# Performance work log

Measured on AMD Instinct MI355X. Metric: run time of the kernel, lower is better.

Reference implementation:

```python
import jax, jax.numpy as jnp
import numpy as np
from jax import lax

D_MODEL = 768
EXPAND = 2
D_INNER = D_MODEL * EXPAND  # 1536
N_STATE = 16
DT_RANK = D_INNER // 16  # 96
K_CONV = 4
B, L = 2, 1024


def setup_inputs() -> dict:
    key = jax.random.key(0)
    ks = jax.random.split(key, 20)
    s = lambda i, shape, scale=0.02: jax.random.normal(ks[i], shape, dtype=jnp.float32) * scale
    # dt_proj bias init (inverse softplus of dt in [0.001, 0.1])
    def dt_bias(k):
        dt = jnp.exp(jax.random.uniform(k, (D_INNER,)) * (np.log(0.1) - np.log(0.001)) + np.log(0.001))
        return dt + jnp.log(-jnp.expm1(-dt))
    A_log = jnp.log(jnp.arange(1, N_STATE + 1, dtype=jnp.float32))[None, :] * jnp.ones((D_INNER, 1), jnp.float32)
    inp = {
        "u": jax.random.normal(ks[0], (B, L, D_MODEL), dtype=jnp.float32),
        "norm_w": jnp.ones((D_MODEL,), jnp.float32),
        "norm_b": jnp.zeros((D_MODEL,), jnp.float32),
        "fwd_in_w": s(1, (2 * D_INNER, D_MODEL)),
        "fwd_conv_w": s(2, (D_INNER, 1, K_CONV), 0.1),
        "fwd_conv_b": jnp.zeros((D_INNER,), jnp.float32),
        "fwd_A_log": A_log,
        "fwd_xproj_w": s(3, (DT_RANK + 2 * N_STATE, D_INNER)),
        "fwd_dt_w": s(4, (D_INNER, DT_RANK)),
        "fwd_dt_b": dt_bias(ks[5]),
        "fwd_D": jnp.ones((D_INNER,), jnp.float32),
        "bwd_in_w": s(6, (2 * D_INNER, D_MODEL)),
        "bwd_conv_w": s(7, (D_INNER, 1, K_CONV), 0.1),
        "bwd_conv_b": jnp.zeros((D_INNER,), jnp.float32),
        "bwd_A_log": A_log,
        "bwd_xproj_w": s(8, (DT_RANK + 2 * N_STATE, D_INNER)),
        "bwd_dt_w": s(9, (D_INNER, DT_RANK)),
        "bwd_dt_b": dt_bias(ks[10]),
        "bwd_D": jnp.ones((D_INNER,), jnp.float32),
        "out_w": s(11, (D_MODEL, 2 * D_INNER)),
    }
    return inp


def _layernorm(x, w, b, eps=1e-5):
    mu = jnp.mean(x, axis=-1, keepdims=True)
    var = jnp.mean(jnp.square(x - mu), axis=-1, keepdims=True)
    return (x - mu) * lax.rsqrt(var + eps) * w + b


def _dw_causal_conv(x, w, b):
    # x: (B, L, D); torch Conv1d(pad=k-1, groups=D) then trim to L == left-pad causal conv
    xc = jnp.transpose(x, (0, 2, 1))  # (B, D, L)
    y = lax.conv_general_dilated(xc, w, window_strides=(1,),
                                 padding=[(K_CONV - 1, 0)],
                                 feature_group_count=D_INNER,
                                 dimension_numbers=('NCH', 'OIH', 'NCH'))
    return jnp.transpose(y + b[None, :, None], (0, 2, 1))


def _ssm(x, A_log, xproj_w, dt_w, dt_b, Dp):
    # x: (B, L, D)
    x_dbl = x @ xproj_w.T  # (B, L, dt_rank + 2N)
    dt_raw = x_dbl[..., :DT_RANK]
    B_sel = x_dbl[..., DT_RANK:DT_RANK + N_STATE]   # (B, L, N)
    C_sel = x_dbl[..., DT_RANK + N_STATE:]           # (B, L, N)
    dt = jax.nn.softplus(dt_raw @ dt_w.T + dt_b)      # (B, L, D)
    A = -jnp.exp(A_log)                               # (D, N)
    A_bar = jnp.exp(dt[..., None] * A)                # (B, L, D, N)
    Bu = (dt * x)[..., None] * B_sel[:, :, None, :]   # (B, L, D, N)
    # linear recurrence h_t = A_bar_t * h_{t-1} + Bu_t via associative scan
    def combine(c1, c2):
        a1, b1 = c1
        a2, b2 = c2
        return a1 * a2, a2 * b1 + b2
    _, h = lax.associative_scan(combine, (A_bar, Bu), axis=1)
    y = jnp.einsum('bldn,bln->bld', h, C_sel)
    return y + x * Dp


def _branch(u, in_w, conv_w, conv_b, A_log, xproj_w, dt_w, dt_b, Dp, reverse):
    if reverse:
        u = u[:, ::-1]
    xz = u @ in_w.T
    x, z = xz[..., :D_INNER], xz[..., D_INNER:]
    x = jax.nn.silu(_dw_causal_conv(x, conv_w, conv_b))
    x = _ssm(x, A_log, xproj_w, dt_w, dt_b, Dp)
    x = x * jax.nn.silu(z)
    if reverse:
        x = x[:, ::-1]
    return x


def reference(u, norm_w, norm_b,
              fwd_in_w, fwd_conv_w, fwd_conv_b, fwd_A_log, fwd_xproj_w, fwd_dt_w, fwd_dt_b, fwd_D,
              bwd_in_w, bwd_conv_w, bwd_conv_b, bwd_A_log, bwd_xproj_w, bwd_dt_w, bwd_dt_b, bwd_D,
              out_w):
    residual = u
    un = _layernorm(u, norm_w, norm_b)
    x_fwd = _branch(un, fwd_in_w, fwd_conv_w, fwd_conv_b, fwd_A_log, fwd_xproj_w, fwd_dt_w, fwd_dt_b, fwd_D, False)
    x_bwd = _branch(un, bwd_in_w, bwd_conv_w, bwd_conv_b, bwd_A_log, bwd_xproj_w, bwd_dt_w, bwd_dt_b, bwd_D, True)
    x = jnp.concatenate([x_fwd, x_bwd], axis=-1) @ out_w.T
    return x + residual
```

## Files before the change

kernel.cpp:

```cpp
#include <hip/hip_runtime.h>
#include <hip/hip_bf16.h>

#define D_MODEL 768
#define D_INNER 1536
#define N_STATE 16
#define DT_RANK 96
#define KCONV   4
#define Bv      2
#define Lv      1024
#define MROWS   (Bv*Lv)

typedef __attribute__((ext_vector_type(8))) short bf16x8;
typedef __attribute__((ext_vector_type(4))) float f32x4;

__device__ __forceinline__ void gll16(const void* g, void* l) {
    __builtin_amdgcn_global_load_lds(
        (const __attribute__((address_space(1))) void*)g,
        (__attribute__((address_space(3))) void*)l, 16, 0, 0);
}

__device__ __forceinline__ unsigned short f2bf(float f) {
    unsigned u = __builtin_bit_cast(unsigned, f);
    u += 0x7fffu + ((u >> 16) & 1u);
    return (unsigned short)(u >> 16);
}

__global__ __launch_bounds__(256)
void ln_kernel(const float* __restrict__ u, const float* __restrict__ w,
               const float* __restrict__ bvec, unsigned short* __restrict__ o)
{
    int row = blockIdx.x;
    const float* x = u + (size_t)row * D_MODEL;
    int t = threadIdx.x;
    float v0 = x[t], v1 = x[t + 256], v2 = x[t + 512];
    float s  = v0 + v1 + v2;
    float s2 = v0*v0 + v1*v1 + v2*v2;
    for (int off = 32; off; off >>= 1) {
        s  += __shfl_down(s, off);
        s2 += __shfl_down(s2, off);
    }
    __shared__ float rs[4], rs2[4];
    __shared__ float mu_s, rstd_s;
    int wid = t >> 6, lane = t & 63;
    if (lane == 0) { rs[wid] = s; rs2[wid] = s2; }
    __syncthreads();
    if (t == 0) {
        float S  = rs[0] + rs[1] + rs[2] + rs[3];
        float S2 = rs2[0] + rs2[1] + rs2[2] + rs2[3];
        float mu = S / (float)D_MODEL;
        float var = S2 / (float)D_MODEL - mu * mu;
        mu_s = mu;
        rstd_s = rsqrtf(var + 1e-5f);
    }
    __syncthreads();
    float mu = mu_s, r = rstd_s;
    unsigned short* orow = o + (size_t)row * D_MODEL;
    orow[t]       = f2bf((v0 - mu) * r * w[t]       + bvec[t]);
    orow[t + 256] = f2bf((v1 - mu) * r * w[t + 256] + bvec[t + 256]);
    orow[t + 512] = f2bf((v2 - mu) * r * w[t + 512] + bvec[t + 512]);
}

__global__ __launch_bounds__(256)
void f2b(const float* __restrict__ in, unsigned short* __restrict__ o, int n4)
{
    int i = blockIdx.x * 256 + threadIdx.x;
    if (i < n4) {
        float4 v = ((const float4*)in)[i];
        ushort4 r;
        r.x = f2bf(v.x); r.y = f2bf(v.y); r.z = f2bf(v.z); r.w = f2bf(v.w);
        ((ushort4*)o)[i] = r;
    }
}

__global__ __launch_bounds__(256)
void gemm_mfma(const unsigned short* __restrict__ A, int revA, int Lr,
               const unsigned short* __restrict__ W,
               const float* __restrict__ res,
               float* __restrict__ C,
               int M, int N, int K)
{
    __shared__ unsigned short As[128 * 32];
    __shared__ unsigned short Bs[128 * 32];
    const int tid = threadIdx.x;
    const int m0 = blockIdx.y * 128, n0 = blockIdx.x * 128;
    const int lane = tid & 63;
    const int w  = tid >> 6;
    const int wr = w >> 1, wc = w & 1;
    const int lm = lane & 15, lk = lane >> 4;

    const int srow = tid >> 2;
    const int skq  = (tid & 3) * 8;
    int arow0 = m0 + srow, arow1 = m0 + srow + 64;
    if (revA) {
        arow0 = (arow0 / Lr) * Lr + (Lr - 1 - arow0 % Lr);
        arow1 = (arow1 / Lr) * Lr + (Lr - 1 - arow1 % Lr);
    }
    const unsigned short* a0 = A + (size_t)arow0 * K + skq;
    const unsigned short* a1 = A + (size_t)arow1 * K + skq;
    const unsigned short* w0 = W + (size_t)(n0 + srow) * K + skq;
    const unsigned short* w1 = W + (size_t)(n0 + srow + 64) * K + skq;

    f32x4 acc[4][4] = {};

    for (int k0 = 0; k0 < K; k0 += 32) {
        __syncthreads();
        gll16(a0 + k0, &As[tid * 8]);
        gll16(a1 + k0, &As[2048 + tid * 8]);
        gll16(w0 + k0, &Bs[tid * 8]);
        gll16(w1 + k0, &Bs[2048 + tid * 8]);
        __syncthreads();

        bf16x8 af[4], bfr[4];
        #pragma unroll
        for (int i = 0; i < 4; i++) {
            af[i]  = *(const bf16x8*)&As[(wr * 64 + i * 16 + lm) * 32 + lk * 8];
            bfr[i] = *(const bf16x8*)&Bs[(wc * 64 + i * 16 + lm) * 32 + lk * 8];
        }
        #pragma unroll
        for (int i = 0; i < 4; i++)
            #pragma unroll
            for (int j = 0; j < 4; j++)
                acc[i][j] = __builtin_amdgcn_mfma_f32_16x16x32_bf16(af[i], bfr[j], acc[i][j], 0, 0, 0);
    }

    #pragma unroll
    for (int i = 0; i < 4; i++) {
        #pragma unroll
        for (int j = 0; j < 4; j++) {
            int row = m0 + wr * 64 + i * 16 + lk * 4;
            int col = n0 + wc * 64 + j * 16 + lm;
            #pragma unroll
            for (int r = 0; r < 4; r++) {
                float v = acc[i][j][r];
                if (res) v += res[(size_t)(row + r) * N + col];
                C[(size_t)(row + r) * N + col] = v;
            }
        }
    }
}

__global__ __launch_bounds__(256)
void conv_silu(const float* __restrict__ xz, const float* __restrict__ w,
               const float* __restrict__ bias, float* __restrict__ xo,
               unsigned short* __restrict__ xbf)
{
    int t  = blockIdx.x * 256 + threadIdx.x;
    int d  = t % D_INNER;
    int lc = (t / D_INNER) % (Lv / 8);
    int b  = t / (D_INNER * (Lv / 8));
    int l0 = lc * 8;
    const float* src = xz + (size_t)b * Lv * (2 * D_INNER) + d;
    float w0 = w[d*4], w1 = w[d*4+1], w2 = w[d*4+2], w3 = w[d*4+3];
    float bb = bias[d];
    float v[11];
    #pragma unroll
    for (int j = 0; j < 11; j++) {
        int l = l0 - 3 + j;
        v[j] = (l >= 0) ? src[(size_t)l * (2 * D_INNER)] : 0.f;
    }
    size_t base = ((size_t)b * Lv + l0) * D_INNER + d;
    #pragma unroll
    for (int j = 0; j < 8; j++) {
        float a = bb + w0*v[j] + w1*v[j+1] + w2*v[j+2] + w3*v[j+3];
        a = a / (1.f + __expf(-a));
        xo[base + (size_t)j * D_INNER] = a;
        xbf[base + (size_t)j * D_INNER] = f2bf(a);
    }
}

__global__ __launch_bounds__(256)
void gemm_bt(const float* __restrict__ A, int lda, int aoff, int revA, int Lr,
             const float* __restrict__ W, int ldw,
             const float* __restrict__ bias, int act,
             const float* __restrict__ res, int ldres,
             float* __restrict__ C, int ldc,
             int M, int N, int K)
{
    __shared__ float As[16][64];
    __shared__ float Ws[16][64];
    const int t  = threadIdx.x;
    const int m0 = blockIdx.y * 64, n0 = blockIdx.x * 64;
    const int lr = t >> 2, kq = t & 3;
    int am = m0 + lr;
    if (revA) { int b = am / Lr, l = am % Lr; am = b * Lr + (Lr - 1 - l); }
    const float* Ap = A + (size_t)am * lda + aoff + kq * 4;
    const float* Wp = W + (size_t)(n0 + lr) * ldw + kq * 4;
    const int ty = t >> 4, tx = t & 15;
    float acc[4][4] = {};
    for (int k0 = 0; k0 < K; k0 += 16) {
        float4 av = *(const float4*)(Ap + k0);
        float4 wv = *(const float4*)(Wp + k0);
        __syncthreads();
        As[kq*4+0][lr] = av.x; As[kq*4+1][lr] = av.y;
        As[kq*4+2][lr] = av.z; As[kq*4+3][lr] = av.w;
        Ws[kq*4+0][lr] = wv.x; Ws[kq*4+1][lr] = wv.y;
        Ws[kq*4+2][lr] = wv.z; Ws[kq*4+3][lr] = wv.w;
        __syncthreads();
        #pragma unroll
        for (int k = 0; k < 16; k++) {
            float4 ra = *(const float4*)&As[k][ty << 2];
            float4 rw = *(const float4*)&Ws[k][tx << 2];
            float a4[4] = {ra.x, ra.y, ra.z, ra.w};
            float w4[4] = {rw.x, rw.y, rw.z, rw.w};
            #pragma unroll
            for (int i = 0; i < 4; i++)
                #pragma unroll
                for (int j = 0; j < 4; j++)
                    acc[i][j] = fmaf(a4[i], w4[j], acc[i][j]);
        }
    }
    #pragma unroll
    for (int i = 0; i < 4; i++) {
        int row = m0 + (ty << 2) + i;
        #pragma unroll
        for (int j = 0; j < 4; j++) {
            int col = n0 + (tx << 2) + j;
            float v = acc[i][j];
            if (bias) v += bias[col];
            if (act == 2) v = (v > 20.f) ? v : log1pf(__expf(v));
            if (res)  v += res[(size_t)row * ldres + col];
            C[(size_t)row * ldc + col] = v;
        }
    }
}

#define SCH  64
#define SNC  (Lv/SCH)
#define PADL 68

template<int CTRL>
__device__ __forceinline__ float dpp_ror_add(float v) {
    int vi = __builtin_bit_cast(int, v);
    int mv = __builtin_amdgcn_update_dpp(vi, vi, CTRL, 0xf, 0xf, true);
    return v + __builtin_bit_cast(float, mv);
}

__global__ __launch_bounds__(128)
void scan_kernel(const float* __restrict__ xF,  const float* __restrict__ dtF,
                 const float* __restrict__ xdF, const float* __restrict__ xzF,
                 const float* __restrict__ AlF, const float* __restrict__ DFp,
                 const float* __restrict__ xB,  const float* __restrict__ dtB,
                 const float* __restrict__ xdB, const float* __restrict__ xzB,
                 const float* __restrict__ AlB, const float* __restrict__ DBp,
                 unsigned short* __restrict__ ycat)
{
    const int br = blockIdx.z;
    const int bb = blockIdx.y;
    const int d0 = blockIdx.x * 8;

    const float* x    = br ? xB  : xF;
    const float* dt   = br ? dtB : dtF;
    const float* xd   = br ? xdB : xdF;
    const float* xz   = br ? xzB : xzF;
    const float* Alog = br ? AlB : AlF;
    const float* Dp   = br ? DBp : DFp;

    __shared__ float xs [2][8][PADL];
    __shared__ float dts[2][8][PADL];
    __shared__ float zs [2][8][PADL];
    __shared__ float Bss[2][16][PADL];
    __shared__ float Css[2][16][PADL];

    const int t = threadIdx.x;
    const int n = t & 15, dloc = t >> 4;

    const float* xg  = x  + (size_t)bb * Lv * D_INNER + d0;
    const float* dtg = dt + (size_t)bb * Lv * D_INNER + d0;
    const float* zg  = xz + (size_t)bb * Lv * (2*D_INNER) + D_INNER + d0;
    const float* bcg = xd + (size_t)bb * Lv * 128;

    const int sl = t >> 1, sdq = (t & 1) * 4;
    const int bl0 = t >> 2,         bq0 = (t & 3) * 4;
    const int bl1 = (t + 128) >> 2, bq1 = ((t + 128) & 3) * 4;

    f32x4 rx, rdt, rz, rb0, rb1, rc0, rc1;

    #define LOADG(c) do {                                                        \
        int l0_ = (c) * SCH;                                                     \
        rx  = *(const f32x4*)(xg  + (size_t)(l0_ + sl) * D_INNER     + sdq);     \
        rdt = *(const f32x4*)(dtg + (size_t)(l0_ + sl) * D_INNER     + sdq);     \
        rz  = *(const f32x4*)(zg  + (size_t)(l0_ + sl) * (2*D_INNER) + sdq);     \
        rb0 = *(const f32x4*)(bcg + (size_t)(l0_ + bl0) * 128 + DT_RANK           + bq0); \
        rb1 = *(const f32x4*)(bcg + (size_t)(l0_ + bl1) * 128 + DT_RANK           + bq1); \
        rc0 = *(const f32x4*)(bcg + (size_t)(l0_ + bl0) * 128 + DT_RANK + N_STATE + bq0); \
        rc1 = *(const f32x4*)(bcg + (size_t)(l0_ + bl1) * 128 + DT_RANK + N_STATE + bq1); \
    } while (0)

    #define WRITEL(p) do {                                                       \
        _Pragma("unroll")                                                        \
        for (int j = 0; j < 4; j++) {                                            \
            xs [p][sdq+j][sl] = rx[j];                                           \
            dts[p][sdq+j][sl] = rdt[j];                                          \
            zs [p][sdq+j][sl] = rz[j];                                           \
            Bss[p][bq0+j][bl0] = rb0[j];                                         \
            Bss[p][bq1+j][bl1] = rb1[j];                                         \
            Css[p][bq0+j][bl0] = rc0[j];                                         \
            Css[p][bq1+j][bl1] = rc1[j];                                         \
        }                                                                        \
    } while (0)

    const float An = -__expf(Alog[(d0 + dloc) * N_STATE + n]);
    const float Dd = Dp[d0 + dloc];
    float h = 0.f;

    LOADG(0);
    WRITEL(0);
    __syncthreads();

    for (int c = 0; c < SNC; ++c) {
        const int p = c & 1;
        if (c + 1 < SNC) LOADG(c + 1);

        float yq[4] = {0.f, 0.f, 0.f, 0.f};
        #pragma unroll
        for (int g = 0; g < 16; ++g) {
            f32x4 xv  = *(const f32x4*)&xs [p][dloc][g*4];
            f32x4 dtv = *(const f32x4*)&dts[p][dloc][g*4];
            f32x4 zv  = *(const f32x4*)&zs [p][dloc][g*4];
            f32x4 bv  = *(const f32x4*)&Bss[p][n][g*4];
            f32x4 cv  = *(const f32x4*)&Css[p][n][g*4];
            #pragma unroll
            for (int j = 0; j < 4; ++j) {
                const int l = g * 4 + j;
                float ab = __expf(dtv[j] * An);
                h = fmaf(ab, h, dtv[j] * xv[j] * bv[j]);
                float contrib = h * cv[j];
                contrib = dpp_ror_add<0x121>(contrib);
                contrib = dpp_ror_add<0x122>(contrib);
                contrib = dpp_ror_add<0x124>(contrib);
                contrib = dpp_ror_add<0x128>(contrib);
                float y = (contrib + xv[j] * Dd)
                        * (zv[j] * __builtin_amdgcn_rcpf(1.f + __expf(-zv[j])));
                if ((l & 15) == n) yq[l >> 4] = y;
            }
        }

        if (c + 1 < SNC) WRITEL(p ^ 1);

        #pragma unroll
        for (int q = 0; q < 4; ++q) {
            int gl = c * SCH + q * 16 + n;
            int lo = br ? (Lv - 1 - gl) : gl;
            ycat[((size_t)bb * Lv + lo) * (2*D_INNER) + br * D_INNER + d0 + dloc] = f2bf(yq[q]);
        }
        __syncthreads();
    }
    #undef LOADG
    #undef WRITEL
}

extern "C" void kernel_launch(void* const* d_in, const int* in_sizes, int n_in,
                              void* d_out, int out_size, void* d_ws, size_t ws_size,
                              hipStream_t stream)
{
    (void)in_sizes; (void)n_in; (void)out_size; (void)ws_size;
    const float* u        = (const float*)d_in[0];
    const float* norm_w   = (const float*)d_in[1];
    const float* norm_b   = (const float*)d_in[2];
    const float* f_in_w   = (const float*)d_in[3];
    const float* f_conv_w = (const float*)d_in[4];
    const float* f_conv_b = (const float*)d_in[5];
    const float* f_Alog   = (const float*)d_in[6];
    const float* f_xproj  = (const float*)d_in[7];
    const float* f_dt_w   = (const float*)d_in[8];
    const float* f_dt_b   = (const float*)d_in[9];
    const float* f_D      = (const float*)d_in[10];
    const float* b_in_w   = (const float*)d_in[11];
    const float* b_conv_w = (const float*)d_in[12];
    const float* b_conv_b = (const float*)d_in[13];
    const float* b_Alog   = (const float*)d_in[14];
    const float* b_xproj  = (const float*)d_in[15];
    const float* b_dt_w   = (const float*)d_in[16];
    const float* b_dt_b   = (const float*)d_in[17];
    const float* b_D      = (const float*)d_in[18];
    const float* out_w    = (const float*)d_in[19];
    float* out = (float*)d_out;

    float* ws = (float*)d_ws;
    float* p = ws;
    unsigned short* un_bf = (unsigned short*)p;  p += (size_t)MROWS * D_MODEL;
    float* xz_f   = p;  p += (size_t)MROWS * 2 * D_INNER;
    float* xz_b   = p;  p += (size_t)MROWS * 2 * D_INNER;
    float* x_f    = p;  p += (size_t)MROWS * D_INNER;
    float* x_b    = p;  p += (size_t)MROWS * D_INNER;
    unsigned short* xbf_f = (unsigned short*)p;  p += (size_t)MROWS * D_INNER / 2;
    unsigned short* xbf_b = (unsigned short*)p;  p += (size_t)MROWS * D_INNER / 2;
    float* xdbl_f = p;  p += (size_t)MROWS * 128;
    float* xdbl_b = p;  p += (size_t)MROWS * 128;
    float* dt_f   = p;  p += (size_t)MROWS * D_INNER;
    float* dt_b_  = p;  p += (size_t)MROWS * D_INNER;
    unsigned short* yc_bf = (unsigned short*)p;  p += (size_t)MROWS * D_INNER;
    unsigned short* fw_bf = (unsigned short*)p;  p += (size_t)D_INNER * D_MODEL;
    unsigned short* bw_bf = (unsigned short*)p;  p += (size_t)D_INNER * D_MODEL;
    unsigned short* xwf_bf = (unsigned short*)p; p += (size_t)64 * D_INNER;
    unsigned short* xwb_bf = (unsigned short*)p; p += (size_t)64 * D_INNER;
    unsigned short* ow_bf = (unsigned short*)p;  p += (size_t)D_MODEL * D_INNER;

    ln_kernel<<<MROWS, 256, 0, stream>>>(u, norm_w, norm_b, un_bf);

    f2b<<<(2*D_INNER*D_MODEL/4 + 255)/256, 256, 0, stream>>>(f_in_w, fw_bf, 2*D_INNER*D_MODEL/4);
    f2b<<<(2*D_INNER*D_MODEL/4 + 255)/256, 256, 0, stream>>>(b_in_w, bw_bf, 2*D_INNER*D_MODEL/4);
    f2b<<<(128*D_INNER/4 + 255)/256, 256, 0, stream>>>(f_xproj, xwf_bf, 128*D_INNER/4);
    f2b<<<(128*D_INNER/4 + 255)/256, 256, 0, stream>>>(b_xproj, xwb_bf, 128*D_INNER/4);
    f2b<<<(D_MODEL*2*D_INNER/4 + 255)/256, 256, 0, stream>>>(out_w, ow_bf, D_MODEL*2*D_INNER/4);

    gemm_mfma<<<dim3(2*D_INNER/128, MROWS/128), 256, 0, stream>>>(
        un_bf, 0, Lv, fw_bf, nullptr, xz_f, MROWS, 2*D_INNER, D_MODEL);
    gemm_mfma<<<dim3(2*D_INNER/128, MROWS/128), 256, 0, stream>>>(
        un_bf, 1, Lv, bw_bf, nullptr, xz_b, MROWS, 2*D_INNER, D_MODEL);

    int convBlocks = (Bv * (Lv/8) * D_INNER) / 256;
    conv_silu<<<convBlocks, 256, 0, stream>>>(xz_f, f_conv_w, f_conv_b, x_f, xbf_f);
    conv_silu<<<convBlocks, 256, 0, stream>>>(xz_b, b_conv_w, b_conv_b, x_b, xbf_b);

    gemm_mfma<<<dim3(1, MROWS/128), 256, 0, stream>>>(
        xbf_f, 0, Lv, xwf_bf, nullptr, xdbl_f, MROWS, 128, D_INNER);
    gemm_mfma<<<dim3(1, MROWS/128), 256, 0, stream>>>(
        xbf_b, 0, Lv, xwb_bf, nullptr, xdbl_b, MROWS, 128, D_INNER);

    gemm_bt<<<dim3(D_INNER/64, MROWS/64), 256, 0, stream>>>(
        xdbl_f, 128, 0, 0, Lv, f_dt_w, DT_RANK, f_dt_b, 2, nullptr, 0,
        dt_f, D_INNER, MROWS, D_INNER, DT_RANK);
    gemm_bt<<<dim3(D_INNER/64, MROWS/64), 256, 0, stream>>>(
        xdbl_b, 128, 0, 0, Lv, b_dt_w, DT_RANK, b_dt_b, 2, nullptr, 0,
        dt_b_, D_INNER, MROWS, D_INNER, DT_RANK);

    scan_kernel<<<dim3(D_INNER/8, Bv, 2), 128, 0, stream>>>(
        x_f, dt_f, xdbl_f, xz_f, f_Alog, f_D,
        x_b, dt_b_, xdbl_b, xz_b, b_Alog, b_D, yc_bf);

    gemm_mfma<<<dim3(D_MODEL/128, MROWS/128), 256, 0, stream>>>(
        yc_bf, 0, Lv, ow_bf, u, out, MROWS, D_MODEL, 2*D_INNER);
}
```

Measured before the change: 519.8 us.

## Split selective scan into chunked three-phase scan; run dt_proj on bf16 MFMA

The single serial scan over the full sequence becomes three kernels. The first computes chunk-local states, outputs and cumulative dt sums for 8 chunks of 128 in parallel. The second propagates chunk-boundary states. The third applies the carried-in state correction and the silu(z) gating. Separately, the fp32 dt_proj GEMM is replaced by the MFMA GEMM, with bias and softplus fused into its epilogue, running on bf16-converted x_dbl and weights. This adds workspace traffic (y_loc, prefix sums, per-chunk states) and bf16 rounding of the dt inputs, in exchange for far more parallelism in the scan.

```diff
diff --git a/kernel.cpp b/kernel.cpp
--- a/kernel.cpp
+++ b/kernel.cpp
@@ -9,6 +9,9 @@
 #define Bv      2
 #define Lv      1024
 #define MROWS   (Bv*Lv)
+#define CH      128
+#define G       (Lv/CH)
+#define PADL    68
 
 typedef __attribute__((ext_vector_type(8))) short bf16x8;
 typedef __attribute__((ext_vector_type(4))) float f32x4;
@@ -23,6 +26,13 @@
     unsigned u = __builtin_bit_cast(unsigned, f);
     u += 0x7fffu + ((u >> 16) & 1u);
     return (unsigned short)(u >> 16);
+}
+
+template<int CTRL>
+__device__ __forceinline__ float dpp_ror_add(float v) {
+    int vi = __builtin_bit_cast(int, v);
+    int mv = __builtin_amdgcn_update_dpp(vi, vi, CTRL, 0xf, 0xf, true);
+    return v + __builtin_bit_cast(float, mv);
 }
 
 __global__ __launch_bounds__(256)
@@ -73,8 +83,9 @@
 }
 
 __global__ __launch_bounds__(256)
-void gemm_mfma(const unsigned short* __restrict__ A, int revA, int Lr,
+void gemm_mfma(const unsigned short* __restrict__ A, int lda, int revA, int Lr,
                const unsigned short* __restrict__ W,
+               const float* __restrict__ bias, int act,
                const float* __restrict__ res,
                float* __restrict__ C,
                int M, int N, int K)
@@ -95,8 +106,8 @@
         arow0 = (arow0 / Lr) * Lr + (Lr - 1 - arow0 % Lr);
         arow1 = (arow1 / Lr) * Lr + (Lr - 1 - arow1 % Lr);
     }
-    const unsigned short* a0 = A + (size_t)arow0 * K + skq;
-    const unsigned short* a1 = A + (size_t)arow1 * K + skq;
+    const unsigned short* a0 = A + (size_t)arow0 * lda + skq;
+    const unsigned short* a1 = A + (size_t)arow1 * lda + skq;
     const unsigned short* w0 = W + (size_t)(n0 + srow) * K + skq;
     const unsigned short* w1 = W + (size_t)(n0 + srow + 64) * K + skq;
 
@@ -132,7 +143,9 @@
             #pragma unroll
             for (int r = 0; r < 4; r++) {
                 float v = acc[i][j][r];
-                if (res) v += res[(size_t)(row + r) * N + col];
+                if (bias) v += bias[col];
+                if (act == 2) v = (v > 20.f) ? v : log1pf(__expf(v));
+                if (res)  v += res[(size_t)(row + r) * N + col];
                 C[(size_t)(row + r) * N + col] = v;
             }
         }
@@ -168,130 +181,58 @@
     }
 }
 
-__global__ __launch_bounds__(256)
-void gemm_bt(const float* __restrict__ A, int lda, int aoff, int revA, int Lr,
-             const float* __restrict__ W, int ldw,
-             const float* __restrict__ bias, int act,
-             const float* __restrict__ res, int ldres,
-             float* __restrict__ C, int ldc,
-             int M, int N, int K)
-{
-    __shared__ float As[16][64];
-    __shared__ float Ws[16][64];
-    const int t  = threadIdx.x;
-    const int m0 = blockIdx.y * 64, n0 = blockIdx.x * 64;
-    const int lr = t >> 2, kq = t & 3;
-    int am = m0 + lr;
-    if (revA) { int b = am / Lr, l = am % Lr; am = b * Lr + (Lr - 1 - l); }
-    const float* Ap = A + (size_t)am * lda + aoff + kq * 4;
-    const float* Wp = W + (size_t)(n0 + lr) * ldw + kq * 4;
-    const int ty = t >> 4, tx = t & 15;
-    float acc[4][4] = {};
-    for (int k0 = 0; k0 < K; k0 += 16) {
-        float4 av = *(const float4*)(Ap + k0);
-        float4 wv = *(const float4*)(Wp + k0);
-        __syncthreads();
-        As[kq*4+0][lr] = av.x; As[kq*4+1][lr] = av.y;
-        As[kq*4+2][lr] = av.z; As[kq*4+3][lr] = av.w;
-        Ws[kq*4+0][lr] = wv.x; Ws[kq*4+1][lr] = wv.y;
-        Ws[kq*4+2][lr] = wv.z; Ws[kq*4+3][lr] = wv.w;
-        __syncthreads();
-        #pragma unroll
-        for (int k = 0; k < 16; k++) {
-            float4 ra = *(const float4*)&As[k][ty << 2];
-            float4 rw = *(const float4*)&Ws[k][tx << 2];
-            float a4[4] = {ra.x, ra.y, ra.z, ra.w};
-            float w4[4] = {rw.x, rw.y, rw.z, rw.w};
-            #pragma unroll
-            for (int i = 0; i < 4; i++)
-                #pragma unroll
-                for (int j = 0; j < 4; j++)
-                    acc[i][j] = fmaf(a4[i], w4[j], acc[i][j]);
-        }
-    }
-    #pragma unroll
-    for (int i = 0; i < 4; i++) {
-        int row = m0 + (ty << 2) + i;
-        #pragma unroll
-        for (int j = 0; j < 4; j++) {
-            int col = n0 + (tx << 2) + j;
-            float v = acc[i][j];
-            if (bias) v += bias[col];
-            if (act == 2) v = (v > 20.f) ? v : log1pf(__expf(v));
-            if (res)  v += res[(size_t)row * ldres + col];
-            C[(size_t)row * ldc + col] = v;
-        }
-    }
-}
-
-#define SCH  64
-#define SNC  (Lv/SCH)
-#define PADL 68
-
-template<int CTRL>
-__device__ __forceinline__ float dpp_ror_add(float v) {
-    int vi = __builtin_bit_cast(int, v);
-    int mv = __builtin_amdgcn_update_dpp(vi, vi, CTRL, 0xf, 0xf, true);
-    return v + __builtin_bit_cast(float, mv);
-}
-
 __global__ __launch_bounds__(128)
-void scan_kernel(const float* __restrict__ xF,  const float* __restrict__ dtF,
-                 const float* __restrict__ xdF, const float* __restrict__ xzF,
-                 const float* __restrict__ AlF, const float* __restrict__ DFp,
-                 const float* __restrict__ xB,  const float* __restrict__ dtB,
-                 const float* __restrict__ xdB, const float* __restrict__ xzB,
-                 const float* __restrict__ AlB, const float* __restrict__ DBp,
-                 unsigned short* __restrict__ ycat)
+void scan1(const float* __restrict__ xF, float* __restrict__ dtF,
+           const float* __restrict__ xdF, const float* __restrict__ AlF,
+           const float* __restrict__ DFp,
+           const float* __restrict__ xB, float* __restrict__ dtB,
+           const float* __restrict__ xdB, const float* __restrict__ AlB,
+           const float* __restrict__ DBp,
+           float* __restrict__ y_loc, float* __restrict__ h_end)
 {
     const int br = blockIdx.z;
-    const int bb = blockIdx.y;
+    const int bb = blockIdx.y >> 3, g = blockIdx.y & 7;
     const int d0 = blockIdx.x * 8;
 
     const float* x    = br ? xB  : xF;
-    const float* dt   = br ? dtB : dtF;
+    float*       dtp  = br ? dtB : dtF;
     const float* xd   = br ? xdB : xdF;
-    const float* xz   = br ? xzB : xzF;
     const float* Alog = br ? AlB : AlF;
     const float* Dp   = br ? DBp : DFp;
 
     __shared__ float xs [2][8][PADL];
-    __shared__ float dts[2][8][PADL];
-    __shared__ float zs [2][8][PADL];
+    __shared__ float dls[2][8][PADL];
     __shared__ float Bss[2][16][PADL];
     __shared__ float Css[2][16][PADL];
 
     const int t = threadIdx.x;
     const int n = t & 15, dloc = t >> 4;
 
-    const float* xg  = x  + (size_t)bb * Lv * D_INNER + d0;
-    const float* dtg = dt + (size_t)bb * Lv * D_INNER + d0;
-    const float* zg  = xz + (size_t)bb * Lv * (2*D_INNER) + D_INNER + d0;
-    const float* bcg = xd + (size_t)bb * Lv * 128;
+    const float* xg  = x   + ((size_t)bb * Lv + g * CH) * D_INNER + d0;
+    float*       dtg = dtp + ((size_t)bb * Lv + g * CH) * D_INNER + d0;
+    const float* bcg = xd  + ((size_t)bb * Lv + g * CH) * 128;
 
     const int sl = t >> 1, sdq = (t & 1) * 4;
     const int bl0 = t >> 2,         bq0 = (t & 3) * 4;
     const int bl1 = (t + 128) >> 2, bq1 = ((t + 128) & 3) * 4;
 
-    f32x4 rx, rdt, rz, rb0, rb1, rc0, rc1;
-
-    #define LOADG(c) do {                                                        \
-        int l0_ = (c) * SCH;                                                     \
-        rx  = *(const f32x4*)(xg  + (size_t)(l0_ + sl) * D_INNER     + sdq);     \
-        rdt = *(const f32x4*)(dtg + (size_t)(l0_ + sl) * D_INNER     + sdq);     \
-        rz  = *(const f32x4*)(zg  + (size_t)(l0_ + sl) * (2*D_INNER) + sdq);     \
+    f32x4 rx, rdt, rb0, rb1, rc0, rc1;
+
+    #define LOADG1(c) do {                                                       \
+        int l0_ = (c) * 64;                                                      \
+        rx  = *(const f32x4*)(xg  + (size_t)(l0_ + sl) * D_INNER + sdq);         \
+        rdt = *(const f32x4*)(dtg + (size_t)(l0_ + sl) * D_INNER + sdq);         \
         rb0 = *(const f32x4*)(bcg + (size_t)(l0_ + bl0) * 128 + DT_RANK           + bq0); \
         rb1 = *(const f32x4*)(bcg + (size_t)(l0_ + bl1) * 128 + DT_RANK           + bq1); \
         rc0 = *(const f32x4*)(bcg + (size_t)(l0_ + bl0) * 128 + DT_RANK + N_STATE + bq0); \
         rc1 = *(const f32x4*)(bcg + (size_t)(l0_ + bl1) * 128 + DT_RANK + N_STATE + bq1); \
     } while (0)
 
-    #define WRITEL(p) do {                                                       \
+    #define WRITEL1(p) do {                                                      \
         _Pragma("unroll")                                                        \
         for (int j = 0; j < 4; j++) {                                            \
             xs [p][sdq+j][sl] = rx[j];                                           \
-            dts[p][sdq+j][sl] = rdt[j];                                          \
-            zs [p][sdq+j][sl] = rz[j];                                           \
+            dls[p][sdq+j][sl] = rdt[j];                                          \
             Bss[p][bq0+j][bl0] = rb0[j];                                         \
             Bss[p][bq1+j][bl1] = rb1[j];                                         \
             Css[p][bq0+j][bl0] = rc0[j];                                         \
@@ -301,52 +242,180 @@
 
     const float An = -__expf(Alog[(d0 + dloc) * N_STATE + n]);
     const float Dd = Dp[d0 + dloc];
-    float h = 0.f;
-
-    LOADG(0);
-    WRITEL(0);
+    float h = 0.f, srun = 0.f;
+
+    LOADG1(0);
+    WRITEL1(0);
     __syncthreads();
 
-    for (int c = 0; c < SNC; ++c) {
-        const int p = c & 1;
-        if (c + 1 < SNC) LOADG(c + 1);
-
-        float yq[4] = {0.f, 0.f, 0.f, 0.f};
-        #pragma unroll
-        for (int g = 0; g < 16; ++g) {
-            f32x4 xv  = *(const f32x4*)&xs [p][dloc][g*4];
-            f32x4 dtv = *(const f32x4*)&dts[p][dloc][g*4];
-            f32x4 zv  = *(const f32x4*)&zs [p][dloc][g*4];
-            f32x4 bv  = *(const f32x4*)&Bss[p][n][g*4];
-            f32x4 cv  = *(const f32x4*)&Css[p][n][g*4];
+    for (int c = 0; c < 2; ++c) {
+        const int p = c;
+        if (c == 0) LOADG1(1);
+
+        float yq[4] = {}, Sq[4] = {};
+        #pragma unroll
+        for (int gg = 0; gg < 16; ++gg) {
+            f32x4 xv  = *(const f32x4*)&xs [p][dloc][gg*4];
+            f32x4 dtv = *(const f32x4*)&dls[p][dloc][gg*4];
+            f32x4 bv  = *(const f32x4*)&Bss[p][n][gg*4];
+            f32x4 cv  = *(const f32x4*)&Css[p][n][gg*4];
             #pragma unroll
             for (int j = 0; j < 4; ++j) {
-                const int l = g * 4 + j;
-                float ab = __expf(dtv[j] * An);
-                h = fmaf(ab, h, dtv[j] * xv[j] * bv[j]);
+                const int l = gg * 4 + j;
+                float dtl = dtv[j];
+                float ab = __expf(dtl * An);
+                h = fmaf(ab, h, dtl * xv[j] * bv[j]);
+                srun += dtl;
                 float contrib = h * cv[j];
                 contrib = dpp_ror_add<0x121>(contrib);
                 contrib = dpp_ror_add<0x122>(contrib);
                 contrib = dpp_ror_add<0x124>(contrib);
                 contrib = dpp_ror_add<0x128>(contrib);
-                float y = (contrib + xv[j] * Dd)
-                        * (zv[j] * __builtin_amdgcn_rcpf(1.f + __expf(-zv[j])));
+                float y = contrib + xv[j] * Dd;
+                if ((l & 15) == n) { yq[l >> 4] = y; Sq[l >> 4] = srun; }
+            }
+        }
+        if (c == 0) WRITEL1(1);
+
+        #pragma unroll
+        for (int q = 0; q < 4; ++q) {
+            int lc2 = c * 64 + q * 16 + n;
+            int gl  = g * CH + lc2;
+            y_loc[((size_t)(br*Bv + bb) * Lv + gl) * D_INNER + d0 + dloc] = yq[q];
+            dtg[(size_t)lc2 * D_INNER + dloc] = Sq[q];
+        }
+        __syncthreads();
+    }
+    h_end[(((size_t)(br*Bv + bb) * G + g) * D_INNER + d0 + dloc) * 16 + n] = h;
+    #undef LOADG1
+    #undef WRITEL1
+}
+
+__global__ __launch_bounds__(256)
+void scan2(const float* __restrict__ SF, const float* __restrict__ SB,
+           const float* __restrict__ AlF, const float* __restrict__ AlB,
+           const float* __restrict__ h_end, float* __restrict__ h0buf)
+{
+    int idx = blockIdx.x * 256 + threadIdx.x;
+    int n = idx & 15;
+    int rest = idx >> 4;
+    int d  = rest % D_INNER;
+    int bbr = rest / D_INNER;
+    int bb = bbr & 1, br = bbr >> 1;
+
+    const float* S    = br ? SB  : SF;
+    const float* Alog = br ? AlB : AlF;
+    float An = -__expf(Alog[d * N_STATE + n]);
+
+    float h0 = 0.f;
+    #pragma unroll
+    for (int g = 0; g < G; ++g) {
+        size_t base = (((size_t)(br*Bv + bb) * G + g) * D_INNER + d) * 16 + n;
+        h0buf[base] = h0;
+        float Send = S[((size_t)bb * Lv + g * CH + CH - 1) * D_INNER + d];
+        h0 = __expf(An * Send) * h0 + h_end[base];
+    }
+}
+
+__global__ __launch_bounds__(128)
+void scan3(const float* __restrict__ SF, const float* __restrict__ xdF,
+           const float* __restrict__ xzF, const float* __restrict__ AlF,
+           const float* __restrict__ SB, const float* __restrict__ xdB,
+           const float* __restrict__ xzB, const float* __restrict__ AlB,
+           const float* __restrict__ y_loc, const float* __restrict__ h0buf,
+           unsigned short* __restrict__ ycat)
+{
+    const int br = blockIdx.z;
+    const int bb = blockIdx.y >> 3, g = blockIdx.y & 7;
+    const int d0 = blockIdx.x * 8;
+
+    const float* S    = br ? SB  : SF;
+    const float* xd   = br ? xdB : xdF;
+    const float* xz   = br ? xzB : xzF;
+    const float* Alog = br ? AlB : AlF;
+
+    __shared__ float Ss [2][8][PADL];
+    __shared__ float zs [2][8][PADL];
+    __shared__ float ys [2][8][PADL];
+    __shared__ float Css[2][16][PADL];
+
+    const int t = threadIdx.x;
+    const int n = t & 15, dloc = t >> 4;
+
+    const float* Sg  = S  + ((size_t)bb * Lv + g * CH) * D_INNER + d0;
+    const float* zg  = xz + ((size_t)bb * Lv + g * CH) * (2*D_INNER) + D_INNER + d0;
+    const float* yg  = y_loc + ((size_t)(br*Bv + bb) * Lv + g * CH) * D_INNER + d0;
+    const float* bcg = xd + ((size_t)bb * Lv + g * CH) * 128;
+
+    const int sl = t >> 1, sdq = (t & 1) * 4;
+    const int bl0 = t >> 2,         bq0 = (t & 3) * 4;
+    const int bl1 = (t + 128) >> 2, bq1 = ((t + 128) & 3) * 4;
+
+    f32x4 rS, rz, ry, rc0, rc1;
+
+    #define LOADG3(c) do {                                                       \
+        int l0_ = (c) * 64;                                                      \
+        rS = *(const f32x4*)(Sg + (size_t)(l0_ + sl) * D_INNER + sdq);           \
+        rz = *(const f32x4*)(zg + (size_t)(l0_ + sl) * (2*D_INNER) + sdq);       \
+        ry = *(const f32x4*)(yg + (size_t)(l0_ + sl) * D_INNER + sdq);           \
+        rc0 = *(const f32x4*)(bcg + (size_t)(l0_ + bl0) * 128 + DT_RANK + N_STATE + bq0); \
+        rc1 = *(const f32x4*)(bcg + (size_t)(l0_ + bl1) * 128 + DT_RANK + N_STATE + bq1); \
+    } while (0)
+
+    #define WRITEL3(p) do {                                                      \
+        _Pragma("unroll")                                                        \
+        for (int j = 0; j < 4; j++) {                                            \
+            Ss[p][sdq+j][sl] = rS[j];                                            \
+            zs[p][sdq+j][sl] = rz[j];                                            \
+            ys[p][sdq+j][sl] = ry[j];                                            \
+            Css[p][bq0+j][bl0] = rc0[j];                                         \
+            Css[p][bq1+j][bl1] = rc1[j];                                         \
+        }                                                                        \
+    } while (0)
+
+    const float An = -__expf(Alog[(d0 + dloc) * N_STATE + n]);
+    const float h0 = h0buf[(((size_t)(br*Bv + bb) * G + g) * D_INNER + d0 + dloc) * 16 + n];
+
+    LOADG3(0);
+    WRITEL3(0);
+    __syncthreads();
+
+    for (int c = 0; c < 2; ++c) {
+        const int p = c;
+        if (c == 0) LOADG3(1);
+
+        float yq[4] = {};
+        #pragma unroll
+        for (int gg = 0; gg < 16; ++gg) {
+            f32x4 Sv = *(const f32x4*)&Ss [p][dloc][gg*4];
+            f32x4 zv = *(const f32x4*)&zs [p][dloc][gg*4];
+            f32x4 yv = *(const f32x4*)&ys [p][dloc][gg*4];
+            f32x4 cv = *(const f32x4*)&Css[p][n][gg*4];
+            #pragma unroll
+            for (int j = 0; j < 4; ++j) {
+                const int l = gg * 4 + j;
+                float corr = cv[j] * __expf(An * Sv[j]) * h0;
+                corr = dpp_ror_add<0x121>(corr);
+                corr = dpp_ror_add<0x122>(corr);
+                corr = dpp_ror_add<0x124>(corr);
+                corr = dpp_ror_add<0x128>(corr);
+                float y = yv[j] + corr;
+                y *= zv[j] * __builtin_amdgcn_rcpf(1.f + __expf(-zv[j]));
                 if ((l & 15) == n) yq[l >> 4] = y;
             }
         }
-
-        if (c + 1 < SNC) WRITEL(p ^ 1);
+        if (c == 0) WRITEL3(1);
 
         #pragma unroll
         for (int q = 0; q < 4; ++q) {
-            int gl = c * SCH + q * 16 + n;
+            int gl = g * CH + c * 64 + q * 16 + n;
             int lo = br ? (Lv - 1 - gl) : gl;
             ycat[((size_t)bb * Lv + lo) * (2*D_INNER) + br * D_INNER + d0 + dloc] = f2bf(yq[q]);
         }
         __syncthreads();
     }
-    #undef LOADG
-    #undef WRITEL
+    #undef LOADG3
+    #undef WRITEL3
 }
 
 extern "C" void kernel_launch(void* const* d_in, const int* in_sizes, int n_in,
@@ -376,8 +445,7 @@
     const float* out_w    = (const float*)d_in[19];
     float* out = (float*)d_out;
 
-    float* ws = (float*)d_ws;
-    float* p = ws;
+    float* p = (float*)d_ws;
     unsigned short* un_bf = (unsigned short*)p;  p += (size_t)MROWS * D_MODEL;
     float* xz_f   = p;  p += (size_t)MROWS * 2 * D_INNER;
     float* xz_b   = p;  p += (size_t)MROWS * 2 * D_INNER;
@@ -395,6 +463,13 @@
     unsigned short* xwf_bf = (unsigned short*)p; p += (size_t)64 * D_INNER;
     unsigned short* xwb_bf = (unsigned short*)p; p += (size_t)64 * D_INNER;
     unsigned short* ow_bf = (unsigned short*)p;  p += (size_t)D_MODEL * D_INNER;
+    float* y_loc  = p;  p += (size_t)2 * MROWS * D_INNER;
+    float* h_end  = p;  p += (size_t)2 * Bv * G * D_INNER * N_STATE;
+    float* h0buf  = p;  p += (size_t)2 * Bv * G * D_INNER * N_STATE;
+    unsigned short* xdbf_f = (unsigned short*)p; p += (size_t)MROWS * 128 / 2;
+    unsigned short* xdbf_b = (unsigned short*)p; p += (size_t)MROWS * 128 / 2;
+    unsigned short* dtwf_bf = (unsigned short*)p; p += (size_t)D_INNER * DT_RANK / 2;
+    unsigned short* dtwb_bf = (unsigned short*)p; p += (size_t)D_INNER * DT_RANK / 2;
 
     ln_kernel<<<MROWS, 256, 0, stream>>>(u, norm_w, norm_b, un_bf);
 
@@ -403,32 +478,39 @@
     f2b<<<(128*D_INNER/4 + 255)/256, 256, 0, stream>>>(f_xproj, xwf_bf, 128*D_INNER/4);
     f2b<<<(128*D_INNER/4 + 255)/256, 256, 0, stream>>>(b_xproj, xwb_bf, 128*D_INNER/4);
     f2b<<<(D_MODEL*2*D_INNER/4 + 255)/256, 256, 0, stream>>>(out_w, ow_bf, D_MODEL*2*D_INNER/4);
+    f2b<<<(D_INNER*DT_RANK/4 + 255)/256, 256, 0, stream>>>(f_dt_w, dtwf_bf, D_INNER*DT_RANK/4);
+    f2b<<<(D_INNER*DT_RANK/4 + 255)/256, 256, 0, stream>>>(b_dt_w, dtwb_bf, D_INNER*DT_RANK/4);
 
     gemm_mfma<<<dim3(2*D_INNER/128, MROWS/128), 256, 0, stream>>>(
-        un_bf, 0, Lv, fw_bf, nullptr, xz_f, MROWS, 2*D_INNER, D_MODEL);
+        un_bf, D_MODEL, 0, Lv, fw_bf, nullptr, 0, nullptr, xz_f, MROWS, 2*D_INNER, D_MODEL);
     gemm_mfma<<<dim3(2*D_INNER/128, MROWS/128), 256, 0, stream>>>(
-        un_bf, 1, Lv, bw_bf, nullptr, xz_b, MROWS, 2*D_INNER, D_MODEL);
+        un_bf, D_MODEL, 1, Lv, bw_bf, nullptr, 0, nullptr, xz_b, MROWS, 2*D_INNER, D_MODEL);
 
     int convBlocks = (Bv * (Lv/8) * D_INNER) / 256;
     conv_silu<<<convBlocks, 256, 0, stream>>>(xz_f, f_conv_w, f_conv_b, x_f, xbf_f);
     conv_silu<<<convBlocks, 256, 0, stream>>>(xz_b, b_conv_w, b_conv_b, x_b, xbf_b);
 
     gemm_mfma<<<dim3(1, MROWS/128), 256, 0, stream>>>(
-        xbf_f, 0, Lv, xwf_bf, nullptr, xdbl_f, MROWS, 128, D_INNER);
+        xbf_f, D_INNER, 0, Lv, xwf_bf, nullptr, 0, nullptr, xdbl_f, MROWS, 128, D_INNER);
     gemm_mfma<<<dim3(1, MROWS/128), 256, 0, stream>>>(
-        xbf_b, 0, Lv, xwb_bf, nullptr, xdbl_b, MROWS, 128, D_INNER);
-
-    gemm_bt<<<dim3(D_INNER/64, MROWS/64), 256, 0, stream>>>(
-        xdbl_f, 128, 0, 0, Lv, f_dt_w, DT_RANK, f_dt_b, 2, nullptr, 0,
-        dt_f, D_INNER, MROWS, D_INNER, DT_RANK);
-    gemm_bt<<<dim3(D_INNER/64, MROWS/64), 256, 0, stream>>>(
-        xdbl_b, 128, 0, 0, Lv, b_dt_w, DT_RANK, b_dt_b, 2, nullptr, 0,
-        dt_b_, D_INNER, MROWS, D_INNER, DT_RANK);
-
-    scan_kernel<<<dim3(D_INNER/8, Bv, 2), 128, 0, stream>>>(
-        x_f, dt_f, xdbl_f, xz_f, f_Alog, f_D,
-        x_b, dt_b_, xdbl_b, xz_b, b_Alog, b_D, yc_bf);
+        xbf_b, D_INNER, 0, Lv, xwb_bf, nullptr, 0, nullptr, xdbl_b, MROWS, 128, D_INNER);
+
+    f2b<<<(MROWS*128/4 + 255)/256, 256, 0, stream>>>(xdbl_f, xdbf_f, MROWS*128/4);
+    f2b<<<(MROWS*128/4 + 255)/256, 256, 0, stream>>>(xdbl_b, xdbf_b, MROWS*128/4);
+    gemm_mfma<<<dim3(D_INNER/128, MROWS/128), 256, 0, stream>>>(
+        xdbf_f, 128, 0, Lv, dtwf_bf, f_dt_b, 2, nullptr, dt_f, MROWS, D_INNER, DT_RANK);
+    gemm_mfma<<<dim3(D_INNER/128, MROWS/128), 256, 0, stream>>>(
+        xdbf_b, 128, 0, Lv, dtwb_bf, b_dt_b, 2, nullptr, dt_b_, MROWS, D_INNER, DT_RANK);
+
+    scan1<<<dim3(D_INNER/8, Bv*G, 2), 128, 0, stream>>>(
+        x_f, dt_f, xdbl_f, f_Alog, f_D,
+        x_b, dt_b_, xdbl_b, b_Alog, b_D, y_loc, h_end);
+    scan2<<<(2*Bv*D_INNER*N_STATE)/256, 256, 0, stream>>>(
+        dt_f, dt_b_, f_Alog, b_Alog, h_end, h0buf);
+    scan3<<<dim3(D_INNER/8, Bv*G, 2), 128, 0, stream>>>(
+        dt_f, xdbl_f, xz_f, f_Alog,
+        dt_b_, xdbl_b, xz_b, b_Alog, y_loc, h0buf, yc_bf);
 
     gemm_mfma<<<dim3(D_MODEL/128, MROWS/128), 256, 0, stream>>>(
-        yc_bf, 0, Lv, ow_bf, u, out, MROWS, D_MODEL, 2*D_INNER);
-}
+        yc_bf, 2*D_INNER, 0, Lv, ow_bf, nullptr, 0, u, out, MROWS, D_MODEL, 2*D_INNER);
+}
```

Result: slower. 622.9 us (+19.8%).
